# Performance work log

Measured on AMD Instinct MI355X. Metric: run time of the kernel, lower is better.

Reference implementation:

```python
import jax, jax.numpy as jnp
import numpy as np
import math

B, CIN, COUT, H, W, K, SDIM = 8, 512, 512, 64, 64, 3, 512
EPS = 1e-8
NEG_SLOPE = 0.2
SCALE = math.sqrt(2.0)


def setup_inputs() -> dict:
    key = jax.random.key(0)
    ks = jax.random.split(key, 7)
    x = jax.random.normal(ks[0], (B, CIN, H, W), jnp.float32)
    style = jax.random.normal(ks[1], (B, SDIM), jnp.float32)
    noise = jax.random.normal(ks[2], (B, 1, H, W), jnp.float32)
    # kernel stored as (kh, kw, Cin, Cout) like keras Conv2D
    fan_in = K * K * CIN
    kernel = jax.random.normal(ks[3], (K, K, CIN, COUT), jnp.float32) / math.sqrt(fan_in)
    style_scale = jax.random.normal(ks[4], (SDIM, COUT), jnp.float32) * 0.02
    bias = jax.random.normal(ks[5], (COUT,), jnp.float32) * 0.01
    noise_weight = jax.random.normal(ks[6], (1,), jnp.float32) * 0.1
    return {"x": x, "style": style, "noise": noise, "kernel": kernel,
            "style_scale": style_scale, "bias": bias, "noise_weight": noise_weight}


def _styled_conv(x, style, noise, kernel, style_scale, bias, noise_weight):
    b = x.shape[0]
    # --- modulation ---
    s = style @ style_scale                              # [B, Cout]
    w = kernel[None] * (s[:, None, None, None, :] + 1.0)  # [B, kh, kw, Cin, Cout]
    # --- demodulation ---
    d = jax.lax.rsqrt(jnp.sum(jnp.square(w), axis=(1, 2, 3)) + EPS)  # [B, Cout]
    w = w * d[:, None, None, None, :]
    # --- per-sample conv via batch-as-groups trick ---
    # weights -> OIHW with O = B*Cout, groups = B
    w_oihw = jnp.transpose(w, (0, 4, 3, 1, 2)).reshape(b * COUT, CIN, K, K)
    x_g = x.reshape(1, b * CIN, H, W)
    out = jax.lax.conv_general_dilated(
        x_g, w_oihw, window_strides=(1, 1), padding="SAME",
        feature_group_count=b,
        dimension_numbers=("NCHW", "OIHW", "NCHW"))
    out = out.reshape(b, COUT, H, W)
    # --- noise injection ---
    out = out + noise_weight[0] * noise                  # noise broadcasts over channels
    # --- fused bias + leaky relu * sqrt(2) ---
    out = jax.nn.leaky_relu(out + bias[None, :, None, None], NEG_SLOPE) * SCALE
    return out


def reference(x, style, noise, kernel, style_scale, bias, noise_weight):
    return _styled_conv(x, style, noise, kernel, style_scale, bias, noise_weight)
```

## Files before the change

kernel.cpp:

```cpp
#include <hip/hip_runtime.h>

#define B_     8
#define CIN_   512
#define COUT_  512
#define HW_    64
#define SDIM_  512
#define NPIX   4096
#define KTOT   4608
#define PADW   66

typedef __attribute__((ext_vector_type(4))) float f32x4;
typedef __attribute__((ext_vector_type(8))) short bf16x8;
typedef __attribute__((ext_vector_type(8))) unsigned short u16x8;

__device__ __forceinline__ float bf2f(unsigned short b) {
    unsigned int u = ((unsigned int)b) << 16;
    return __builtin_bit_cast(float, u);
}
__device__ __forceinline__ unsigned short f2bf(float f) {
    unsigned int u = __builtin_bit_cast(unsigned int, f);
    return (unsigned short)((u + 0x7fffu + ((u >> 16) & 1u)) >> 16);
}
__device__ __forceinline__ float ldin(const void* p, size_t i, int isbf) {
    return isbf ? bf2f(((const unsigned short*)p)[i]) : ((const float*)p)[i];
}

#define GLD16(g, l) __builtin_amdgcn_global_load_lds( \
    (__attribute__((address_space(1))) void*)(g),     \
    (__attribute__((address_space(3))) void*)(l), 16, 0, 0)

__global__ void detect_dtype(const unsigned int* __restrict__ style_u32,
                             int* __restrict__ flag) {
    int t = threadIdx.x;
    unsigned int w = style_u32[t * 4];
    int e = (w >> 7) & 0xFF;
    int isbf = (e >= 110 && e <= 140) ? 1 : 0;
    __shared__ int cnt;
    if (t == 0) cnt = 0;
    __syncthreads();
    atomicAdd(&cnt, isbf);
    __syncthreads();
    if (t == 0) *flag = (cnt >= 128) ? 1 : 0;
}

__global__ void wt_transpose(const void* __restrict__ kin,
                             unsigned short* __restrict__ wt,
                             const int* __restrict__ flag) {
    __shared__ __align__(16) unsigned short tile[64][72];
    int isbf = *flag;
    int t = threadIdx.x;
    int co0 = blockIdx.x * 64;
    int k0  = blockIdx.y * 64;
    int r = t >> 2, c16 = (t & 3) << 4;
    if (isbf) {
        const unsigned short* src = (const unsigned short*)kin + (size_t)(k0 + r) * COUT_ + co0 + c16;
        *(u16x8*)&tile[r][c16]     = *(const u16x8*)src;
        *(u16x8*)&tile[r][c16 + 8] = *(const u16x8*)(src + 8);
    } else {
        const float* src = (const float*)kin + (size_t)(k0 + r) * COUT_ + co0 + c16;
#pragma unroll
        for (int q = 0; q < 4; ++q) {
            f32x4 v = *(const f32x4*)(src + q * 4);
#pragma unroll
            for (int j = 0; j < 4; ++j) tile[r][c16 + q * 4 + j] = f2bf(v[j]);
        }
    }
    __syncthreads();
    int c = t >> 2, r16 = (t & 3) << 4;
    u16x8 w0, w1;
#pragma unroll
    for (int j = 0; j < 8; ++j) { w0[j] = tile[r16 + j][c]; w1[j] = tile[r16 + 8 + j][c]; }
    unsigned short* dst = wt + (size_t)(co0 + c) * KTOT + k0 + r16;
    *(u16x8*)dst       = w0;
    *(u16x8*)(dst + 8) = w1;
}

__global__ void xpose(const void* __restrict__ x,
                      unsigned short* __restrict__ xtp,
                      const int* __restrict__ flag) {
    __shared__ __align__(16) unsigned short tile[64][72];
    int isbf = *flag;
    int t = threadIdx.x;
    int cit = blockIdx.x;
    int y   = blockIdx.y;
    int b   = blockIdx.z;
    int ci_l = t >> 2, xo = (t & 3) << 4;
    size_t srcoff = (((size_t)(b * CIN_ + cit * 64 + ci_l)) * HW_ + y) * HW_ + xo;
    if (isbf) {
        const unsigned short* src = (const unsigned short*)x + srcoff;
        *(u16x8*)&tile[ci_l][xo]     = *(const u16x8*)src;
        *(u16x8*)&tile[ci_l][xo + 8] = *(const u16x8*)(src + 8);
    } else {
        const float* src = (const float*)x + srcoff;
#pragma unroll
        for (int q = 0; q < 4; ++q) {
            f32x4 v = *(const f32x4*)(src + q * 4);
#pragma unroll
            for (int j = 0; j < 4; ++j) tile[ci_l][xo + q * 4 + j] = f2bf(v[j]);
        }
    }
    __syncthreads();
    int xl = t >> 2, cio = (t & 3) << 4;
    u16x8 w0, w1;
#pragma unroll
    for (int j = 0; j < 8; ++j) { w0[j] = tile[cio + j][xl]; w1[j] = tile[cio + 8 + j][xl]; }
    unsigned short* dst =
        xtp + (((size_t)b * PADW + (y + 1)) * PADW + (xl + 1)) * CIN_ + cit * 64 + cio;
    *(u16x8*)dst       = w0;
    *(u16x8*)(dst + 8) = w1;
}

__global__ void mod_kernel(const void* __restrict__ style,
                           const void* __restrict__ sscale,
                           const unsigned short* __restrict__ wt,
                           float* __restrict__ mmod,
                           const int* __restrict__ flag) {
    int isbf = *flag;
    int co = blockIdx.x, t = threadIdx.x;
    int lane = t & 63, wid = t >> 6;
    float k2 = 0.f;
    const unsigned short* wr = wt + (size_t)co * KTOT;
    for (int k = t; k < KTOT; k += 256) { float v = bf2f(wr[k]); k2 += v * v; }
    float sb[B_];
#pragma unroll
    for (int b = 0; b < B_; ++b) sb[b] = 0.f;
    for (int sd = t; sd < SDIM_; sd += 256) {
        float ss = ldin(sscale, (size_t)sd * COUT_ + co, isbf);
#pragma unroll
        for (int b = 0; b < B_; ++b) sb[b] += ldin(style, b * SDIM_ + sd, isbf) * ss;
    }
    __shared__ float red[4][9];
    float vals[9];
    vals[0] = k2;
#pragma unroll
    for (int b = 0; b < B_; ++b) vals[1 + b] = sb[b];
#pragma unroll
    for (int q = 0; q < 9; ++q) {
        float v = vals[q];
        for (int off = 32; off; off >>= 1) v += __shfl_down(v, off);
        if (lane == 0) red[wid][q] = v;
    }
    __syncthreads();
    if (t < B_) {
        int b = t;
        float k2t = red[0][0] + red[1][0] + red[2][0] + red[3][0];
        float s   = red[0][1 + b] + red[1][1 + b] + red[2][1 + b] + red[3][1 + b];
        float sp1 = s + 1.f;
        mmod[b * COUT_ + co] = sp1 * rsqrtf(sp1 * sp1 * k2t + 1e-8f);
    }
}

__global__ __launch_bounds__(512, 2) void conv_gemm(
    const unsigned short* __restrict__ wt,
    const unsigned short* __restrict__ xtp,
    const float* __restrict__ mmod,
    const void* __restrict__ noise,
    const void* __restrict__ bias,
    const void* __restrict__ nwp,
    void* __restrict__ out,
    const int* __restrict__ flag) {
    __shared__ __align__(1024) unsigned short Asm[2][256 * 64];
    __shared__ __align__(1024) unsigned short Bsm[2][256 * 64];
    int isbf = *flag;
    int tid = threadIdx.x;
    int lane = tid & 63, wid = tid >> 6;
    int lr = lane & 15, hi = lane >> 4;
    int wm = wid >> 2, wn = wid & 3;

    int bid = blockIdx.x;
    int swz = (bid & 7) * 32 + (bid >> 3);
    int gy = swz >> 7;
    int nb = swz & 127;
    int b  = nb >> 4;
    int nt = nb & 15;
    int pl0 = nt << 8;
    int h0  = pl0 >> 6;
    int co0 = gy << 8;

    const unsigned short* xb = xtp + (size_t)b * (PADW * PADW * CIN_);

    f32x4 acc[8][4];
#pragma unroll
    for (int i = 0; i < 8; ++i)
#pragma unroll
        for (int j = 0; j < 4; ++j) acc[i][j] = (f32x4){0.f, 0.f, 0.f, 0.f};

    int rsub = lane >> 3;
    int ce_src = ((lane & 7) ^ rsub) << 3;

    auto stage = [&](int tt, int pp) {
        int khw = tt >> 3;
        int kh = khw / 3, kw = khw - kh * 3;
        int ci0 = (tt & 7) << 6;
        const unsigned short* srcA =
            wt + (size_t)(co0 + (wid << 5) + rsub) * KTOT + (tt << 6) + ce_src;
        char* ldA = (char*)&Asm[pp][0] + (wid << 12);
#pragma unroll
        for (int i = 0; i < 4; ++i)
            GLD16(srcA + (size_t)(i << 3) * KTOT, ldA + (i << 10));
        char* ldB = (char*)&Bsm[pp][0] + (wid << 12);
#pragma unroll
        for (int i = 0; i < 4; ++i) {
            int p = (wid << 5) + (i << 3) + rsub;
            int h = h0 + (p >> 6), wc = p & 63;
            const unsigned short* srcB =
                xb + ((size_t)(h + kh) * PADW + (wc + kw)) * CIN_ + ci0 + ce_src;
            GLD16(srcB, ldB + (i << 10));
        }
    };

    stage(0, 0);
    stage(1, 1);
    asm volatile("s_waitcnt vmcnt(8)" ::: "memory");
    __builtin_amdgcn_s_barrier();
    __builtin_amdgcn_sched_barrier(0);

    int swzr = (lane & 7) << 3;
    for (int t = 0; t < 72; ++t) {
        int p = t & 1;
        const unsigned short* As = &Asm[p][0];
        const unsigned short* Bs = &Bsm[p][0];
#pragma unroll
        for (int kk = 0; kk < 2; ++kk) {
            bf16x8 af[8], bf[4];
            int ceb = (kk << 5);
#pragma unroll
            for (int mf = 0; mf < 8; ++mf) {
                int row = (wm << 7) + (mf << 4) + lr;
                af[mf] = *(const bf16x8*)&As[row * 64 + ((ceb + (hi << 3)) ^ swzr)];
            }
#pragma unroll
            for (int nf = 0; nf < 4; ++nf) {
                int row = (wn << 6) + (nf << 4) + lr;
                bf[nf] = *(const bf16x8*)&Bs[row * 64 + ((ceb + (hi << 3)) ^ swzr)];
            }
            __builtin_amdgcn_s_setprio(1);
#pragma unroll
            for (int mf = 0; mf < 8; ++mf)
#pragma unroll
                for (int nf = 0; nf < 4; ++nf)
                    acc[mf][nf] = __builtin_amdgcn_mfma_f32_16x16x32_bf16(
                        af[mf], bf[nf], acc[mf][nf], 0, 0, 0);
            __builtin_amdgcn_s_setprio(0);
        }
        asm volatile("s_waitcnt lgkmcnt(0)" ::: "memory");
        __builtin_amdgcn_sched_barrier(0);
        __builtin_amdgcn_s_barrier();
        if (t < 70) {
            stage(t + 2, p);
            asm volatile("s_waitcnt vmcnt(8)" ::: "memory");
        } else {
            asm volatile("s_waitcnt vmcnt(0)" ::: "memory");
        }
        __builtin_amdgcn_s_barrier();
        __builtin_amdgcn_sched_barrier(0);
    }

    float nw = ldin(nwp, 0, isbf);
    unsigned short* out16 = (unsigned short*)out;
    float* outf = (float*)out;
#pragma unroll
    for (int mf = 0; mf < 8; ++mf) {
        int cobase = co0 + (wm << 7) + (mf << 4) + (hi << 2);
        f32x4 mv = *(const f32x4*)&mmod[b * COUT_ + cobase];
        float bb[4];
#pragma unroll
        for (int r = 0; r < 4; ++r) bb[r] = ldin(bias, cobase + r, isbf);
#pragma unroll
        for (int nf = 0; nf < 4; ++nf) {
            int pix = pl0 + (wn << 6) + (nf << 4) + lr;
            float nv = nw * ldin(noise, b * NPIX + pix, isbf);
#pragma unroll
            for (int r = 0; r < 4; ++r) {
                float v = acc[mf][nf][r] * mv[r] + nv + bb[r];
                v = (v < 0.f ? v * 0.2f : v) * 1.41421356237f;
                size_t oidx = ((size_t)(b * COUT_ + cobase + r)) * NPIX + pix;
                if (isbf) out16[oidx] = f2bf(v);
                else      outf[oidx]  = v;
            }
        }
    }
}

extern "C" void kernel_launch(void* const* d_in, const int* in_sizes, int n_in,
                              void* d_out, int out_size, void* d_ws, size_t ws_size,
                              hipStream_t stream) {
    const void* x      = d_in[0];
    const void* style  = d_in[1];
    const void* noise  = d_in[2];
    const void* kin    = d_in[3];
    const void* sscale = d_in[4];
    const void* bias   = d_in[5];
    const void* nwp    = d_in[6];

    char* ws = (char*)d_ws;
    int* flag = (int*)ws;
    const size_t xtp_off  = 256;
    const size_t xtp_bytes = (size_t)B_ * PADW * PADW * CIN_ * 2;
    const size_t wt_bytes  = (size_t)COUT_ * KTOT * 2;
    unsigned short* xtp = (unsigned short*)(ws + xtp_off);
    unsigned short* wtr = (unsigned short*)(ws + xtp_off + xtp_bytes);
    float* mmod         = (float*)(ws + xtp_off + xtp_bytes + wt_bytes);

    detect_dtype<<<1, 256, 0, stream>>>((const unsigned int*)style, flag);
    hipMemsetAsync(xtp, 0, xtp_bytes, stream);
    wt_transpose<<<dim3(8, 72), 256, 0, stream>>>(kin, wtr, flag);
    xpose<<<dim3(8, 64, 8), 256, 0, stream>>>(x, xtp, flag);
    mod_kernel<<<512, 256, 0, stream>>>(style, sscale, wtr, mmod, flag);
    conv_gemm<<<256, 512, 0, stream>>>(wtr, xtp, mmod, noise, bias, nwp, d_out, flag);
}
```

Baseline: 213.1 us.

## Interleave global-to-LDS staging with MFMA phases and zero only the padding halo

The conv GEMM main loop becomes four phases per k-step. Each phase reads its LDS fragments, issues part of the next tile's global-to-LDS loads, then runs 16 MFMAs. This replaces the single bulk stage-and-wait per iteration and is meant to hide load latency behind compute with finer barrier-separated scheduling. Separately, the full memset of the padded input buffer is replaced by a small kernel that zeroes only the halo border, since the interior is overwritten by the transpose. The tighter barrier and waitcnt choreography risks hazards on the double-buffered LDS if the counts are off.

```diff
diff --git a/kernel.cpp b/kernel.cpp
--- a/kernel.cpp
+++ b/kernel.cpp
@@ -41,6 +41,18 @@
     atomicAdd(&cnt, isbf);
     __syncthreads();
     if (t == 0) *flag = (cnt >= 128) ? 1 : 0;
+}
+
+__global__ void halo_zero(unsigned short* __restrict__ xtp) {
+    int idx = blockIdx.x;
+    int b = blockIdx.y;
+    int y, x;
+    if (idx < 66)       { y = 0;  x = idx; }
+    else if (idx < 132) { y = 65; x = idx - 66; }
+    else if (idx < 196) { x = 0;  y = idx - 131; }
+    else                { x = 65; y = idx - 195; }
+    unsigned int* dst = (unsigned int*)(xtp + (((size_t)b * PADW + y) * PADW + x) * CIN_);
+    dst[threadIdx.x] = 0;
 }
 
 __global__ void wt_transpose(const void* __restrict__ kin,
@@ -187,73 +199,118 @@
 
     int rsub = lane >> 3;
     int ce_src = ((lane & 7) ^ rsub) << 3;
-
-    auto stage = [&](int tt, int pp) {
+    int swzr = (lane & 7) << 3;
+
+    auto stageA = [&](int tt, int pp, int q) {
+        const unsigned short* srcA =
+            wt + (size_t)(co0 + (q << 6) + (wid << 3) + rsub) * KTOT + (tt << 6) + ce_src;
+        GLD16(srcA, (char*)&Asm[pp][0] + (q << 13) + (wid << 10));
+    };
+    auto stageB = [&](int tt, int pp, int q) {
         int khw = tt >> 3;
-        int kh = khw / 3, kw = khw - kh * 3;
+        int kh = (khw >= 6) ? 2 : ((khw >= 3) ? 1 : 0);
+        int kw = khw - kh * 3;
         int ci0 = (tt & 7) << 6;
-        const unsigned short* srcA =
-            wt + (size_t)(co0 + (wid << 5) + rsub) * KTOT + (tt << 6) + ce_src;
-        char* ldA = (char*)&Asm[pp][0] + (wid << 12);
-#pragma unroll
-        for (int i = 0; i < 4; ++i)
-            GLD16(srcA + (size_t)(i << 3) * KTOT, ldA + (i << 10));
-        char* ldB = (char*)&Bsm[pp][0] + (wid << 12);
-#pragma unroll
-        for (int i = 0; i < 4; ++i) {
-            int p = (wid << 5) + (i << 3) + rsub;
-            int h = h0 + (p >> 6), wc = p & 63;
-            const unsigned short* srcB =
-                xb + ((size_t)(h + kh) * PADW + (wc + kw)) * CIN_ + ci0 + ce_src;
-            GLD16(srcB, ldB + (i << 10));
-        }
+        int wc = ((wid << 3) + rsub) & 63;
+        const unsigned short* srcB =
+            xb + ((size_t)(h0 + q + kh) * PADW + (wc + kw)) * CIN_ + ci0 + ce_src;
+        GLD16(srcB, (char*)&Bsm[pp][0] + (q << 13) + (wid << 10));
     };
 
-    stage(0, 0);
-    stage(1, 1);
+#pragma unroll
+    for (int q = 0; q < 4; ++q) { stageA(0, 0, q); stageB(0, 0, q); }
+#pragma unroll
+    for (int q = 0; q < 4; ++q) { stageA(1, 1, q); stageB(1, 1, q); }
     asm volatile("s_waitcnt vmcnt(8)" ::: "memory");
     __builtin_amdgcn_s_barrier();
     __builtin_amdgcn_sched_barrier(0);
 
-    int swzr = (lane & 7) << 3;
     for (int t = 0; t < 72; ++t) {
-        int p = t & 1;
+        int p = t & 1, pn = p ^ 1;
         const unsigned short* As = &Asm[p][0];
         const unsigned short* Bs = &Bsm[p][0];
-#pragma unroll
-        for (int kk = 0; kk < 2; ++kk) {
-            bf16x8 af[8], bf[4];
-            int ceb = (kk << 5);
-#pragma unroll
-            for (int mf = 0; mf < 8; ++mf) {
-                int row = (wm << 7) + (mf << 4) + lr;
-                af[mf] = *(const bf16x8*)&As[row * 64 + ((ceb + (hi << 3)) ^ swzr)];
-            }
-#pragma unroll
-            for (int nf = 0; nf < 4; ++nf) {
-                int row = (wn << 6) + (nf << 4) + lr;
-                bf[nf] = *(const bf16x8*)&Bs[row * 64 + ((ceb + (hi << 3)) ^ swzr)];
-            }
-            __builtin_amdgcn_s_setprio(1);
-#pragma unroll
-            for (int mf = 0; mf < 8; ++mf)
-#pragma unroll
-                for (int nf = 0; nf < 4; ++nf)
-                    acc[mf][nf] = __builtin_amdgcn_mfma_f32_16x16x32_bf16(
-                        af[mf], bf[nf], acc[mf][nf], 0, 0, 0);
-            __builtin_amdgcn_s_setprio(0);
-        }
+        bool sN = (t >= 1 && t <= 70);
+        bool s2 = (t <= 69);
+
+        bf16x8 a0[4], bk0[4];
+#pragma unroll
+        for (int i = 0; i < 4; ++i)
+            a0[i] = *(const bf16x8*)&As[(((wm << 7) + (i << 4) + lr) << 6) + ((hi << 3) ^ swzr)];
+#pragma unroll
+        for (int i = 0; i < 4; ++i)
+            bk0[i] = *(const bf16x8*)&Bs[(((wn << 6) + (i << 4) + lr) << 6) + ((hi << 3) ^ swzr)];
+        if (sN) { stageB(t + 1, pn, 0); stageB(t + 1, pn, 1); }
+        __builtin_amdgcn_sched_barrier(0);
+        __builtin_amdgcn_s_barrier();
         asm volatile("s_waitcnt lgkmcnt(0)" ::: "memory");
         __builtin_amdgcn_sched_barrier(0);
-        __builtin_amdgcn_s_barrier();
-        if (t < 70) {
-            stage(t + 2, p);
-            asm volatile("s_waitcnt vmcnt(8)" ::: "memory");
-        } else {
-            asm volatile("s_waitcnt vmcnt(0)" ::: "memory");
-        }
-        __builtin_amdgcn_s_barrier();
-        __builtin_amdgcn_sched_barrier(0);
+        __builtin_amdgcn_s_setprio(1);
+#pragma unroll
+        for (int mf = 0; mf < 4; ++mf)
+#pragma unroll
+            for (int nf = 0; nf < 4; ++nf)
+                acc[mf][nf] = __builtin_amdgcn_mfma_f32_16x16x32_bf16(a0[mf], bk0[nf], acc[mf][nf], 0, 0, 0);
+        __builtin_amdgcn_s_setprio(0);
+        __builtin_amdgcn_s_barrier();
+
+        bf16x8 a1[4];
+#pragma unroll
+        for (int i = 0; i < 4; ++i)
+            a1[i] = *(const bf16x8*)&As[(((wm << 7) + ((i + 4) << 4) + lr) << 6) + ((hi << 3) ^ swzr)];
+        if (sN) { stageB(t + 1, pn, 2); stageB(t + 1, pn, 3); }
+        __builtin_amdgcn_sched_barrier(0);
+        __builtin_amdgcn_s_barrier();
+        asm volatile("s_waitcnt lgkmcnt(0)" ::: "memory");
+        __builtin_amdgcn_sched_barrier(0);
+        __builtin_amdgcn_s_setprio(1);
+#pragma unroll
+        for (int mf = 0; mf < 4; ++mf)
+#pragma unroll
+            for (int nf = 0; nf < 4; ++nf)
+                acc[mf + 4][nf] = __builtin_amdgcn_mfma_f32_16x16x32_bf16(a1[mf], bk0[nf], acc[mf + 4][nf], 0, 0, 0);
+        __builtin_amdgcn_s_setprio(0);
+        __builtin_amdgcn_s_barrier();
+
+        bf16x8 a2[4], bk1[4];
+#pragma unroll
+        for (int i = 0; i < 4; ++i)
+            a2[i] = *(const bf16x8*)&As[(((wm << 7) + (i << 4) + lr) << 6) + ((32 + (hi << 3)) ^ swzr)];
+#pragma unroll
+        for (int i = 0; i < 4; ++i)
+            bk1[i] = *(const bf16x8*)&Bs[(((wn << 6) + (i << 4) + lr) << 6) + ((32 + (hi << 3)) ^ swzr)];
+        if (sN) { stageA(t + 1, pn, 1); stageA(t + 1, pn, 3); }
+        __builtin_amdgcn_sched_barrier(0);
+        __builtin_amdgcn_s_barrier();
+        asm volatile("s_waitcnt lgkmcnt(0)" ::: "memory");
+        __builtin_amdgcn_sched_barrier(0);
+        __builtin_amdgcn_s_setprio(1);
+#pragma unroll
+        for (int mf = 0; mf < 4; ++mf)
+#pragma unroll
+            for (int nf = 0; nf < 4; ++nf)
+                acc[mf][nf] = __builtin_amdgcn_mfma_f32_16x16x32_bf16(a2[mf], bk1[nf], acc[mf][nf], 0, 0, 0);
+        __builtin_amdgcn_s_setprio(0);
+        __builtin_amdgcn_s_barrier();
+
+        bf16x8 a3[4];
+#pragma unroll
+        for (int i = 0; i < 4; ++i)
+            a3[i] = *(const bf16x8*)&As[(((wm << 7) + ((i + 4) << 4) + lr) << 6) + ((32 + (hi << 3)) ^ swzr)];
+        if (s2) { stageA(t + 2, p, 0); stageA(t + 2, p, 2); }
+        if (t <= 69)      asm volatile("s_waitcnt vmcnt(2)" ::: "memory");
+        else if (t == 70) asm volatile("s_waitcnt vmcnt(0)" ::: "memory");
+        __builtin_amdgcn_sched_barrier(0);
+        __builtin_amdgcn_s_barrier();
+        asm volatile("s_waitcnt lgkmcnt(0)" ::: "memory");
+        __builtin_amdgcn_sched_barrier(0);
+        __builtin_amdgcn_s_setprio(1);
+#pragma unroll
+        for (int mf = 0; mf < 4; ++mf)
+#pragma unroll
+            for (int nf = 0; nf < 4; ++nf)
+                acc[mf + 4][nf] = __builtin_amdgcn_mfma_f32_16x16x32_bf16(a3[mf], bk1[nf], acc[mf + 4][nf], 0, 0, 0);
+        __builtin_amdgcn_s_setprio(0);
+        __builtin_amdgcn_s_barrier();
     }
 
     float nw = ldin(nwp, 0, isbf);
@@ -303,7 +360,7 @@
     float* mmod         = (float*)(ws + xtp_off + xtp_bytes + wt_bytes);
 
     detect_dtype<<<1, 256, 0, stream>>>((const unsigned int*)style, flag);
-    hipMemsetAsync(xtp, 0, xtp_bytes, stream);
+    halo_zero<<<dim3(260, 8), 256, 0, stream>>>(xtp);
     wt_transpose<<<dim3(8, 72), 256, 0, stream>>>(kin, wtr, flag);
     xpose<<<dim3(8, 64, 8), 256, 0, stream>>>(x, xtp, flag);
     mod_kernel<<<512, 256, 0, stream>>>(style, sscale, wtr, mmod, flag);
```

Result: faster. 194.4 us (-8.7%).

## Use 4-wave GEMM blocks with 128x128 warp tiles and single-stage prefetch; zero only halo

Applied to the files above, without the earlier changes.

The conv GEMM block goes from 8 waves to 4. Each wave now computes a 128x128 tile (8x8 MFMA fragments) instead of 128x64, which raises register reuse of the A and B fragments. The prefetch schedule changes from two stages in flight with partial vmcnt waits to loading the next stage before compute and then a full vmcnt(0) wait each iteration, which may expose load latency because fewer waves are available to hide it. The full memset of the padded input buffer is replaced by a small kernel that zeroes only the one-pixel halo, avoiding a large redundant write.

```diff
diff --git a/kernel.cpp b/kernel.cpp
--- a/kernel.cpp
+++ b/kernel.cpp
@@ -41,6 +41,18 @@
     atomicAdd(&cnt, isbf);
     __syncthreads();
     if (t == 0) *flag = (cnt >= 128) ? 1 : 0;
+}
+
+__global__ void halo_zero(unsigned short* __restrict__ xtp) {
+    int idx = blockIdx.x;
+    int b = blockIdx.y;
+    int y, x;
+    if (idx < 66)       { y = 0;  x = idx; }
+    else if (idx < 132) { y = 65; x = idx - 66; }
+    else if (idx < 196) { x = 0;  y = idx - 131; }
+    else                { x = 65; y = idx - 195; }
+    unsigned int* dst = (unsigned int*)(xtp + (((size_t)b * PADW + y) * PADW + x) * CIN_);
+    dst[threadIdx.x] = 0;
 }
 
 __global__ void wt_transpose(const void* __restrict__ kin,
@@ -150,7 +162,7 @@
     }
 }
 
-__global__ __launch_bounds__(512, 2) void conv_gemm(
+__global__ __launch_bounds__(256, 1) void conv_gemm(
     const unsigned short* __restrict__ wt,
     const unsigned short* __restrict__ xtp,
     const float* __restrict__ mmod,
@@ -165,7 +177,7 @@
     int tid = threadIdx.x;
     int lane = tid & 63, wid = tid >> 6;
     int lr = lane & 15, hi = lane >> 4;
-    int wm = wid >> 2, wn = wid & 3;
+    int wm = wid >> 1, wn = wid & 1;
 
     int bid = blockIdx.x;
     int swz = (bid & 7) * 32 + (bid >> 3);
@@ -179,81 +191,70 @@
 
     const unsigned short* xb = xtp + (size_t)b * (PADW * PADW * CIN_);
 
-    f32x4 acc[8][4];
+    f32x4 acc[8][8];
 #pragma unroll
     for (int i = 0; i < 8; ++i)
 #pragma unroll
-        for (int j = 0; j < 4; ++j) acc[i][j] = (f32x4){0.f, 0.f, 0.f, 0.f};
+        for (int j = 0; j < 8; ++j) acc[i][j] = (f32x4){0.f, 0.f, 0.f, 0.f};
 
     int rsub = lane >> 3;
     int ce_src = ((lane & 7) ^ rsub) << 3;
-
-    auto stage = [&](int tt, int pp) {
+    int swzr = (lane & 7) << 3;
+
+    auto stageA = [&](int tt, int pp, int g) {
+        int row0 = (g << 5) + (wid << 3);
+        const unsigned short* srcA =
+            wt + (size_t)(co0 + row0 + rsub) * KTOT + (tt << 6) + ce_src;
+        GLD16(srcA, (char*)&Asm[pp][0] + (row0 << 7));
+    };
+    auto stageB = [&](int tt, int pp, int g) {
         int khw = tt >> 3;
-        int kh = khw / 3, kw = khw - kh * 3;
+        int kh = (khw >= 6) ? 2 : ((khw >= 3) ? 1 : 0);
+        int kw = khw - kh * 3;
         int ci0 = (tt & 7) << 6;
-        const unsigned short* srcA =
-            wt + (size_t)(co0 + (wid << 5) + rsub) * KTOT + (tt << 6) + ce_src;
-        char* ldA = (char*)&Asm[pp][0] + (wid << 12);
-#pragma unroll
-        for (int i = 0; i < 4; ++i)
-            GLD16(srcA + (size_t)(i << 3) * KTOT, ldA + (i << 10));
-        char* ldB = (char*)&Bsm[pp][0] + (wid << 12);
-#pragma unroll
-        for (int i = 0; i < 4; ++i) {
-            int p = (wid << 5) + (i << 3) + rsub;
-            int h = h0 + (p >> 6), wc = p & 63;
-            const unsigned short* srcB =
-                xb + ((size_t)(h + kh) * PADW + (wc + kw)) * CIN_ + ci0 + ce_src;
-            GLD16(srcB, ldB + (i << 10));
-        }
+        int p0 = (g << 5) + (wid << 3);
+        int h = h0 + (p0 >> 6), wc = (p0 & 63) + rsub;
+        const unsigned short* srcB =
+            xb + ((size_t)(h + kh) * PADW + (wc + kw)) * CIN_ + ci0 + ce_src;
+        GLD16(srcB, (char*)&Bsm[pp][0] + (p0 << 7));
     };
 
-    stage(0, 0);
-    stage(1, 1);
-    asm volatile("s_waitcnt vmcnt(8)" ::: "memory");
+#pragma unroll
+    for (int g = 0; g < 8; ++g) { stageA(0, 0, g); stageB(0, 0, g); }
+    asm volatile("s_waitcnt vmcnt(0)" ::: "memory");
     __builtin_amdgcn_s_barrier();
-    __builtin_amdgcn_sched_barrier(0);
-
-    int swzr = (lane & 7) << 3;
+
     for (int t = 0; t < 72; ++t) {
-        int p = t & 1;
+        int p = t & 1, pn = p ^ 1;
         const unsigned short* As = &Asm[p][0];
         const unsigned short* Bs = &Bsm[p][0];
+
+        if (t < 71) {
+#pragma unroll
+            for (int g = 0; g < 8; ++g) { stageA(t + 1, pn, g); stageB(t + 1, pn, g); }
+        }
+
 #pragma unroll
         for (int kk = 0; kk < 2; ++kk) {
-            bf16x8 af[8], bf[4];
-            int ceb = (kk << 5);
-#pragma unroll
-            for (int mf = 0; mf < 8; ++mf) {
-                int row = (wm << 7) + (mf << 4) + lr;
-                af[mf] = *(const bf16x8*)&As[row * 64 + ((ceb + (hi << 3)) ^ swzr)];
-            }
-#pragma unroll
-            for (int nf = 0; nf < 4; ++nf) {
-                int row = (wn << 6) + (nf << 4) + lr;
-                bf[nf] = *(const bf16x8*)&Bs[row * 64 + ((ceb + (hi << 3)) ^ swzr)];
-            }
-            __builtin_amdgcn_s_setprio(1);
+            bf16x8 av[8], bv[8];
+            int ceb = (kk << 5) + (hi << 3);
 #pragma unroll
             for (int mf = 0; mf < 8; ++mf)
-#pragma unroll
-                for (int nf = 0; nf < 4; ++nf)
+                av[mf] = *(const bf16x8*)&As[(((wm << 7) + (mf << 4) + lr) << 6) + (ceb ^ swzr)];
+#pragma unroll
+            for (int nf = 0; nf < 8; ++nf)
+                bv[nf] = *(const bf16x8*)&Bs[(((wn << 7) + (nf << 4) + lr) << 6) + (ceb ^ swzr)];
+#pragma unroll
+            for (int mf = 0; mf < 8; ++mf)
+#pragma unroll
+                for (int nf = 0; nf < 8; ++nf)
                     acc[mf][nf] = __builtin_amdgcn_mfma_f32_16x16x32_bf16(
-                        af[mf], bf[nf], acc[mf][nf], 0, 0, 0);
-            __builtin_amdgcn_s_setprio(0);
-        }
+                        av[mf], bv[nf], acc[mf][nf], 0, 0, 0);
+        }
+
         asm volatile("s_waitcnt lgkmcnt(0)" ::: "memory");
-        __builtin_amdgcn_sched_barrier(0);
+        if (t < 71) asm volatile("s_waitcnt vmcnt(0)" ::: "memory");
         __builtin_amdgcn_s_barrier();
-        if (t < 70) {
-            stage(t + 2, p);
-            asm volatile("s_waitcnt vmcnt(8)" ::: "memory");
-        } else {
-            asm volatile("s_waitcnt vmcnt(0)" ::: "memory");
-        }
-        __builtin_amdgcn_s_barrier();
-        __builtin_amdgcn_sched_barrier(0);
     }
 
     float nw = ldin(nwp, 0, isbf);
@@ -267,8 +268,8 @@
 #pragma unroll
         for (int r = 0; r < 4; ++r) bb[r] = ldin(bias, cobase + r, isbf);
 #pragma unroll
-        for (int nf = 0; nf < 4; ++nf) {
-            int pix = pl0 + (wn << 6) + (nf << 4) + lr;
+        for (int nf = 0; nf < 8; ++nf) {
+            int pix = pl0 + (wn << 7) + (nf << 4) + lr;
             float nv = nw * ldin(noise, b * NPIX + pix, isbf);
 #pragma unroll
             for (int r = 0; r < 4; ++r) {
@@ -303,9 +304,9 @@
     float* mmod         = (float*)(ws + xtp_off + xtp_bytes + wt_bytes);
 
     detect_dtype<<<1, 256, 0, stream>>>((const unsigned int*)style, flag);
-    hipMemsetAsync(xtp, 0, xtp_bytes, stream);
+    halo_zero<<<dim3(260, 8), 256, 0, stream>>>(xtp);
     wt_transpose<<<dim3(8, 72), 256, 0, stream>>>(kin, wtr, flag);
     xpose<<<dim3(8, 64, 8), 256, 0, stream>>>(x, xtp, flag);
     mod_kernel<<<512, 256, 0, stream>>>(style, sscale, wtr, mmod, flag);
-    conv_gemm<<<256, 512, 0, stream>>>(wtr, xtp, mmod, noise, bias, nwp, d_out, flag);
-}
+    conv_gemm<<<256, 256, 0, stream>>>(wtr, xtp, mmod, noise, bias, nwp, d_out, flag);
+}
```

After: 272.5 us. 1.28x slower.
